# Kernel optimization log

Hardware: AMD Instinct MI355X
Metric: run time of the kernel (lower is better)

## Reference

```python
import jax, jax.numpy as jnp
import numpy as np

B, F, N, E, T = 8, 16, 1024, 256, 64
ALPHA = 0.2        # LeakyReLU negative slope
NEG = -9.0e15      # masking value used by the torch code


def setup_inputs() -> dict:
    key = jax.random.key(0)
    ks = jax.random.split(key, 9)
    x = jax.random.normal(ks[0], (B, F, N, T), dtype=jnp.float32)
    mask = (jax.random.uniform(ks[1], (B, F, N, T)) > 0.2).astype(jnp.float32)
    # binary incidence matrix [n_nodes, n_edges]; guarantee every hyperedge
    # has at least one incident node (avoids div-by-zero / empty softmax)
    inc = (jax.random.uniform(ks[2], (N, E)) < 0.05).astype(jnp.float32)
    inc = inc.at[0, :].set(1.0)
    h0 = jax.random.normal(ks[3], (1, N), dtype=jnp.float32)      # initial node state row
    h1 = jax.random.normal(ks[4], (E, 1), dtype=jnp.float32)      # initial edge state
    bias = jax.random.uniform(ks[5], (N,), dtype=jnp.float32)     # THGAT.bias (d_model == N)
    weight = jax.random.uniform(ks[6], (2 * F + 1,), dtype=jnp.float32)  # [3*d_in-ish, 1] proj
    weight2 = jax.random.uniform(ks[7], (E, E), dtype=jnp.float32) / E   # edge mixing
    a = jax.random.uniform(ks[8], (2,), dtype=jnp.float32)        # GAT attention vector
    return {"x": x, "mask": mask, "incidence": inc, "h0": h0, "h1": h1,
            "bias": bias, "weight": weight, "weight2": weight2, "a": a}


def _thgat_step(x_s, m_s, n_s, h_e, incidence, bias, weight, weight2, a):
    # x_s, m_s: [B,F,N]; n_s: [B,1,N]; h_e: [B,E,1]
    x_cat = jnp.concatenate([x_s, m_s, n_s], axis=1)          # [B,2F+1,N]
    xn = jnp.einsum('bcn,c->bn', x_cat, weight) + bias         # node feature (scalar per node)
    deg = jnp.sum(incidence, axis=0)                           # [E] hyperedge degree
    edge = (xn @ incidence) / deg                              # [B,E] mean of incident nodes
    edge = edge @ weight2                                      # [B,E]
    # pairwise GAT score at nonzero (n,e) pairs; computed densely then masked,
    # identical math to torch's gather -> sparse_coo -> to_dense path
    s = jax.nn.leaky_relu(xn[:, :, None] * a[0] + edge[:, None, :] * a[1], ALPHA)  # [B,N,E]
    time_e = h_e[:, :, 0] + edge                               # agg_type='sum': pri_e + edge
    s = s + time_e[:, None, :]
    att = jnp.where(incidence[None] > 0, s, NEG)
    attn = jax.nn.softmax(att, axis=1)                         # softmax over nodes per edge
    node = jnp.einsum('bne,be->bn', attn, edge)                # aggregate edge feats to nodes
    return node[:, None, :], edge[:, :, None]                  # [B,1,N], [B,E,1]


def reference(x, mask, incidence, h0, h1, bias, weight, weight2, a):
    n0 = jnp.broadcast_to(h0[None], (B, 1, N))
    e0 = jnp.broadcast_to(h1[None], (B, E, 1))
    xs = jnp.moveaxis(x, -1, 0)     # [T,B,F,N]
    ms = jnp.moveaxis(mask, -1, 0)

    def step(carry, inp):
        n_s, h_e = carry
        x_s, m_s = inp
        node, edge = _thgat_step(x_s, m_s, n_s, h_e, incidence, bias, weight, weight2, a)
        return (node, edge), node[:, 0, :]

    _, nodes = jax.lax.scan(step, (n0, e0), (xs, ms))
    return jnp.moveaxis(nodes, 0, 1)  # [B,T,N] imputations per timestep
```

## Files before the change

### kernel.cpp

```cpp
#include <hip/hip_runtime.h>

#define Bq 8
#define Fq 16
#define Nq 1024
#define Eq 256
#define Tq 64
constexpr float ALPHAq = 0.2f;
constexpr int NNZCAP = 32768;
constexpr int MAXJE  = 20;
constexpr int NNZW2  = 20480;
constexpr int DUMP0  = NNZW2;
constexpr int WVLTOT = NNZW2 + 1024;

__device__ __forceinline__ float qswap1(float x) {
  return __int_as_float(__builtin_amdgcn_mov_dpp(__float_as_int(x), 0xB1, 0xF, 0xF, true));
}
__device__ __forceinline__ float qswap2(float x) {
  return __int_as_float(__builtin_amdgcn_mov_dpp(__float_as_int(x), 0x4E, 0xF, 0xF, true));
}

__global__ __launch_bounds__(256) void k_cntB(const float* __restrict__ inc,
                                              int* __restrict__ gcnt,
                                              int* __restrict__ ncnt) {
  const int i = blockIdx.x, e = threadIdx.x;
  const int base = i * 64;
  int c = 0;
  for (int r = 0; r < 64; ++r) c += (inc[(size_t)(base + r) * Eq + e] > 0.f) ? 1 : 0;
  gcnt[i * Eq + e] = c;
  if (i < 4) {
    const int n = i * 256 + e;
    const float* row = inc + (size_t)n * Eq;
    int cn = 0;
    for (int k = 0; k < Eq; ++k) cn += (row[k] > 0.f) ? 1 : 0;
    ncnt[n] = cn;
  }
}

__global__ __launch_bounds__(1024) void k_prefB(const int* __restrict__ gcnt,
                                                const int* __restrict__ ncnt,
                                                int* __restrict__ g_ptr,
                                                int* __restrict__ goff,
                                                int* __restrict__ tlp,
                                                int* __restrict__ tlp2) {
  __shared__ int tot[Eq];
  __shared__ int sptr[Eq + 1];
  __shared__ int sn[Nq];
  __shared__ int snp[Nq + 1];
  __shared__ int snp2[Nq + 1];
  const int tid = threadIdx.x;
  if (tid < Eq) { int s = 0; for (int i = 0; i < 16; ++i) s += gcnt[i * Eq + tid]; tot[tid] = s; }
  sn[tid] = ncnt[tid];
  __syncthreads();
  if (tid == 0) { int s = 0; for (int j = 0; j < Eq; ++j) { sptr[j] = s; s += tot[j]; } sptr[Eq] = s; }
  if (tid == 1) { int s = 0; for (int i = 0; i < Nq; ++i) { snp[i] = s; s += sn[i]; } snp[Nq] = s; }
  if (tid == 2) { int s = 0; for (int i = 0; i < Nq; ++i) { snp2[i] = s; s += (sn[i] + 3) & ~3; } snp2[Nq] = s; }
  __syncthreads();
  if (tid <= Eq) g_ptr[tid] = sptr[tid];
  tlp[tid] = snp[tid];
  tlp2[tid] = snp2[tid];
  if (tid == 0) { tlp[Nq] = snp[Nq]; tlp2[Nq] = snp2[Nq]; }
  if (tid < Eq) {
    int run = sptr[tid];
    for (int i = 0; i < 16; ++i) { goff[i * Eq + tid] = run; run += gcnt[i * Eq + tid]; }
  }
}

__global__ __launch_bounds__(256) void k_fillB(const float* __restrict__ inc,
                                               const int* __restrict__ goff,
                                               const int* __restrict__ tlp,
                                               unsigned short* __restrict__ g_nodes,
                                               unsigned short* __restrict__ tle_g) {
  const int i = blockIdx.x, e = threadIdx.x;
  const int base = i * 64;
  int w = goff[i * Eq + e];
  for (int r = 0; r < 64; ++r) {
    const int n = base + r;
    if (inc[(size_t)n * Eq + e] > 0.f) { if (w < NNZCAP) g_nodes[w] = (unsigned short)n; ++w; }
  }
  if (i < 4) {
    const int n = i * 256 + e;
    const float* row = inc + (size_t)n * Eq;
    int wn = tlp[n];
    for (int k = 0; k < Eq; ++k)
      if (row[k] > 0.f) { if (wn < NNZCAP) tle_g[wn] = (unsigned short)k; ++wn; }
  }
}

__global__ __launch_bounds__(256) void k_prep(const int* __restrict__ g_ptr,
                                              const unsigned short* __restrict__ g_nodes,
                                              const int* __restrict__ tlp_g,
                                              const int* __restrict__ tlp2_g,
                                              const unsigned short* __restrict__ tle_g,
                                              unsigned* __restrict__ tbl_g,
                                              unsigned short* __restrict__ wpos_g) {
  const int t = blockIdx.x * 256 + threadIdx.x;
  const int e = t >> 2, sub = t & 3;
  const int p0 = g_ptr[e], p1 = g_ptr[e + 1];
  int j = 0;
  for (int pos = p0 + sub; pos < p1; pos += 4, ++j) {
    const int n = (int)g_nodes[pos];
    int lo = tlp_g[n], hi = tlp_g[n + 1];
    while (lo < hi) { int mid = (lo + hi) >> 1; if ((int)tle_g[mid] < e) lo = mid + 1; else hi = mid; }
    int wp = tlp2_g[n] + (lo - tlp_g[n]);
    if (wp >= NNZW2) wp = DUMP0 + t;
    wpos_g[pos] = (unsigned short)wp;
    if (j < MAXJE) tbl_g[j * Nq + t] = ((unsigned)wp << 16) | (unsigned)n;
  }
  for (; j < MAXJE; ++j)
    tbl_g[j * Nq + t] = ((unsigned)(DUMP0 + t) << 16) | (unsigned)Nq;
}

__global__ __launch_bounds__(256) void k_xnp(const float* __restrict__ x,
                                             const float* __restrict__ mask,
                                             const float* __restrict__ weight,
                                             const float* __restrict__ bias,
                                             float* __restrict__ xnpT) {
  __shared__ float accs[64][65];
  const int wg = blockIdx.x;
  const int b = wg >> 4;
  const int n0 = (wg & 15) << 6;
  const int lane = threadIdx.x & 63;
  const int w = threadIdx.x >> 6;
  float a[16];
#pragma unroll
  for (int i = 0; i < 16; ++i) a[i] = 0.f;
  for (int f = 0; f < Fq; ++f) {
    const float wf = weight[f], wm = weight[Fq + f];
#pragma unroll
    for (int ii = 0; ii < 16; ++ii) {
      const int i = w + ii * 4;
      const size_t base = ((size_t)(b * Fq + f) * Nq + n0 + i) * Tq + lane;
      a[ii] += x[base] * wf + mask[base] * wm;
    }
  }
#pragma unroll
  for (int ii = 0; ii < 16; ++ii) accs[w + ii * 4][lane] = a[ii];
  __syncthreads();
  const float bl = bias[n0 + lane];
#pragma unroll
  for (int jj = 0; jj < 16; ++jj) {
    const int tt = w + jj * 4;
    xnpT[((size_t)b * Tq + tt) * Nq + n0 + lane] = accs[lane][tt] + bl;
  }
}

__global__ __attribute__((amdgpu_flat_work_group_size(1024, 1024), amdgpu_waves_per_eu(4, 4)))
void k_recur(
    const float* __restrict__ xnpT, const float* __restrict__ w2,
    const int* __restrict__ g_ptr, const unsigned short* __restrict__ g_nodes,
    const unsigned short* __restrict__ wpos_g,
    const int* __restrict__ tlp_g, const int* __restrict__ tlp2_g,
    const unsigned* __restrict__ tbl_g,
    const float* __restrict__ h0,
    const float* __restrict__ weight, const float* __restrict__ a_vec,
    float* __restrict__ out) {
  __shared__ __align__(16) float wvl[WVLTOT];
  __shared__ float xnl[Nq + 4];
  __shared__ __align__(16) float epp[4 * 72];

  const int b = blockIdx.x;
  const int tid = threadIdx.x;
  const int e = tid >> 2;
  const int sub = tid & 3;
  const float w32 = weight[2 * Fq];
  const float a0 = a_vec[0], a1 = a_vec[1];

  for (int i = tid; i < WVLTOT; i += 1024) wvl[i] = 0.f;

  float xn_reg = xnpT[(size_t)b * Tq * Nq + tid] + w32 * h0[tid];
  xnl[tid] = xn_reg;
  if (tid == 0) xnl[Nq] = 0.f;

  unsigned uj[MAXJE];
#pragma unroll
  for (int j = 0; j < MAXJE; ++j) uj[j] = tbl_g[j * Nq + tid];

  float w2r[64];
#pragma unroll
  for (int kk = 0; kk < 64; ++kk)
    w2r[kk] = w2[(size_t)(sub * 64 + kk) * Eq + e];

  const int p0 = g_ptr[e], p1 = g_ptr[e + 1];
  const float degf = (float)(p1 - p0);
  const int tail0 = p0 + sub + 4 * MAXJE;
  const int q0v = tlp2_g[tid] >> 2;
  const int degn = tlp_g[tid + 1] - tlp_g[tid];
  const int iters = (tid == 0) ? 0 : ((degn + 3) >> 2);
  __syncthreads();

  float xv[MAXJE];

  for (int t = 0; t < Tq; ++t) {
    const float xnext = xnpT[((size_t)b * Tq + (t + 1 < Tq ? t + 1 : t)) * Nq + tid];

    float v = 0.f;
    float mxv = -3.0e38f;
#pragma unroll
    for (int j = 0; j < MAXJE; ++j) {
      const int n = (int)(uj[j] & 0xffffu);
      const float xx = xnl[n];
      v += xx;
      const float val = (n < Nq) ? xx : -1.0e30f;
      xv[j] = val;
      mxv = fmaxf(mxv, val);
    }
    for (int pos = tail0; pos < p1; pos += 4) {
      const float xx = xnl[(int)g_nodes[pos]];
      v += xx;
      mxv = fmaxf(mxv, xx);
    }
    v += qswap1(v);
    v += qswap2(v);
    mxv = fmaxf(mxv, qswap1(mxv));
    mxv = fmaxf(mxv, qswap2(mxv));
    if (sub == 0) epp[(e >> 6) * 72 + (e & 63)] = v / degf;
    __syncthreads();

    float acc = 0.f;
#pragma unroll
    for (int k = 0; k < 16; ++k) {
      const float4 epv = *reinterpret_cast<const float4*>(&epp[sub * 72 + (k << 2)]);
      acc += w2r[k * 4 + 0] * epv.x + w2r[k * 4 + 1] * epv.y +
             w2r[k * 4 + 2] * epv.z + w2r[k * 4 + 3] * epv.w;
    }
    acc += qswap1(acc);
    acc += qswap2(acc);
    const float edge2 = acc;
    const float e2a1 = edge2 * a1;
    const float sm = mxv * a0 + e2a1;
    const float mx = fmaxf(sm, ALPHAq * sm);

    float Zs = 0.f;
#pragma unroll
    for (int j = 0; j < MAXJE; ++j) {
      const float s = xv[j] * a0 + e2a1;
      const float p = __expf(fmaxf(s, ALPHAq * s) - mx);
      xv[j] = p;
      Zs += p;
    }
    for (int pos = tail0; pos < p1; pos += 4) {
      const float s = xnl[(int)g_nodes[pos]] * a0 + e2a1;
      Zs += __expf(fmaxf(s, ALPHAq * s) - mx);
    }
    Zs += qswap1(Zs);
    Zs += qswap2(Zs);
    const float we = edge2 / Zs;

#pragma unroll
    for (int j = 0; j < MAXJE; ++j)
      wvl[uj[j] >> 16] = xv[j] * we;
    for (int pos = tail0; pos < p1; pos += 4) {
      const float s = xnl[(int)g_nodes[pos]] * a0 + e2a1;
      wvl[(int)wpos_g[pos]] = __expf(fmaxf(s, ALPHAq * s) - mx) * we;
    }
    __syncthreads();

    float nv = 0.f;
    if (tid < 64) {
      const float4 w4 = reinterpret_cast<const float4*>(wvl)[tid];
      float q = w4.x + w4.y + w4.z + w4.w;
#pragma unroll
      for (int m = 32; m > 0; m >>= 1) q += __shfl_xor(q, m);
      if (tid == 0) nv = q;
    }
    for (int i = 0; i < iters; ++i) {
      const float4 w4 = reinterpret_cast<const float4*>(wvl)[q0v + i];
      nv += w4.x + w4.y + w4.z + w4.w;
    }

    out[((size_t)b * Tq + t) * Nq + tid] = nv;
    xn_reg = xnext + w32 * nv;
    xnl[tid] = xn_reg;
    __syncthreads();
  }
}

extern "C" void kernel_launch(void* const* d_in, const int* in_sizes, int n_in,
                              void* d_out, int out_size, void* d_ws, size_t ws_size,
                              hipStream_t stream) {
  (void)in_sizes; (void)n_in; (void)out_size; (void)ws_size;
  const float* x      = (const float*)d_in[0];
  const float* mask   = (const float*)d_in[1];
  const float* inc    = (const float*)d_in[2];
  const float* h0     = (const float*)d_in[3];
  const float* bias   = (const float*)d_in[5];
  const float* weight = (const float*)d_in[6];
  const float* w2     = (const float*)d_in[7];
  const float* avec   = (const float*)d_in[8];
  float* out = (float*)d_out;

  char* ws = (char*)d_ws;
  size_t off = 0;
  auto alloc = [&](size_t bytes) { void* p = ws + off; off += (bytes + 255) & ~(size_t)255; return p; };
  int*            g_ptr   = (int*)alloc((Eq + 1) * 4);
  int*            gcnt    = (int*)alloc(16 * Eq * 4);
  int*            goff    = (int*)alloc(16 * Eq * 4);
  unsigned short* g_nodes = (unsigned short*)alloc((size_t)NNZCAP * 2);
  int*            ncnt    = (int*)alloc(Nq * 4);
  int*            tlp_g   = (int*)alloc((Nq + 1) * 4);
  int*            tlp2_g  = (int*)alloc((Nq + 1) * 4);
  unsigned short* tle_g   = (unsigned short*)alloc((size_t)NNZCAP * 2);
  unsigned short* wpos_g  = (unsigned short*)alloc((size_t)NNZCAP * 2);
  unsigned*       tbl_g   = (unsigned*)alloc((size_t)MAXJE * Nq * 4);
  float*          xnpT    = (float*)alloc((size_t)Bq * Tq * Nq * 4);

  k_cntB <<<16, 256, 0, stream>>>(inc, gcnt, ncnt);
  k_prefB<<<1, 1024, 0, stream>>>(gcnt, ncnt, g_ptr, goff, tlp_g, tlp2_g);
  k_fillB<<<16, 256, 0, stream>>>(inc, goff, tlp_g, g_nodes, tle_g);
  k_prep <<<4, 256, 0, stream>>>(g_ptr, g_nodes, tlp_g, tlp2_g, tle_g, tbl_g, wpos_g);
  k_xnp  <<<128, 256, 0, stream>>>(x, mask, weight, bias, xnpT);
  k_recur<<<Bq, 1024, 0, stream>>>(xnpT, w2, g_ptr, g_nodes, wpos_g, tlp_g, tlp2_g,
                                   tbl_g, h0, weight, avec, out);
}
```

Baseline: 549.3 us.

## Sort hyperedges by degree and skip unused padded slots per wave

Hyperedges are ranked by degree in the prefix kernel, and each thread quad is mapped to an edge through that ranking. Edges with similar degree therefore share a wavefront. The recurrence computes a wave-uniform maximum slot count and skips padded MAXJE slots in the gather, exp and scatter loops. This cuts wasted LDS loads and exps in the latency-bound per-timestep loop, at the cost of an extra indirection, a scalar branch per slot, and an O(E²) rank computation during setup.

```diff
diff --git a/kernel.cpp b/kernel.cpp
--- a/kernel.cpp
+++ b/kernel.cpp
@@ -41,7 +41,8 @@
                                                 int* __restrict__ g_ptr,
                                                 int* __restrict__ goff,
                                                 int* __restrict__ tlp,
-                                                int* __restrict__ tlp2) {
+                                                int* __restrict__ tlp2,
+                                                unsigned short* __restrict__ eq_g) {
   __shared__ int tot[Eq];
   __shared__ int sptr[Eq + 1];
   __shared__ int sn[Nq];
@@ -63,6 +64,15 @@
     int run = sptr[tid];
     for (int i = 0; i < 16; ++i) { goff[i * Eq + tid] = run; run += gcnt[i * Eq + tid]; }
   }
+  if (tid < Eq) {
+    const int d = tot[tid];
+    int r = 0;
+    for (int e2 = 0; e2 < Eq; ++e2) {
+      const int d2 = tot[e2];
+      r += (d2 > d) || (d2 == d && e2 < tid);
+    }
+    eq_g[r] = (unsigned short)tid;
+  }
 }
 
 __global__ __launch_bounds__(256) void k_fillB(const float* __restrict__ inc,
@@ -91,10 +101,12 @@
                                               const int* __restrict__ tlp_g,
                                               const int* __restrict__ tlp2_g,
                                               const unsigned short* __restrict__ tle_g,
+                                              const unsigned short* __restrict__ eq_g,
                                               unsigned* __restrict__ tbl_g,
                                               unsigned short* __restrict__ wpos_g) {
   const int t = blockIdx.x * 256 + threadIdx.x;
-  const int e = t >> 2, sub = t & 3;
+  const int q = t >> 2, sub = t & 3;
+  const int e = (int)eq_g[q];
   const int p0 = g_ptr[e], p1 = g_ptr[e + 1];
   int j = 0;
   for (int pos = p0 + sub; pos < p1; pos += 4, ++j) {
@@ -150,7 +162,7 @@
     const int* __restrict__ g_ptr, const unsigned short* __restrict__ g_nodes,
     const unsigned short* __restrict__ wpos_g,
     const int* __restrict__ tlp_g, const int* __restrict__ tlp2_g,
-    const unsigned* __restrict__ tbl_g,
+    const unsigned* __restrict__ tbl_g, const unsigned short* __restrict__ eq_g,
     const float* __restrict__ h0,
     const float* __restrict__ weight, const float* __restrict__ a_vec,
     float* __restrict__ out) {
@@ -160,8 +172,9 @@
 
   const int b = blockIdx.x;
   const int tid = threadIdx.x;
-  const int e = tid >> 2;
+  const int q = tid >> 2;
   const int sub = tid & 3;
+  const int e = (int)eq_g[q];
   const float w32 = weight[2 * Fq];
   const float a0 = a_vec[0], a1 = a_vec[1];
 
@@ -181,11 +194,19 @@
     w2r[kk] = w2[(size_t)(sub * 64 + kk) * Eq + e];
 
   const int p0 = g_ptr[e], p1 = g_ptr[e + 1];
-  const float degf = (float)(p1 - p0);
+  const int deg = p1 - p0;
+  const float degf = (float)deg;
   const int tail0 = p0 + sub + 4 * MAXJE;
   const int q0v = tlp2_g[tid] >> 2;
   const int degn = tlp_g[tid + 1] - tlp_g[tid];
   const int iters = (tid == 0) ? 0 : ((degn + 3) >> 2);
+
+  int cnt = (deg - sub + 3) >> 2;
+  int cm = cnt;
+#pragma unroll
+  for (int m = 1; m <= 32; m <<= 1) { const int o = __shfl_xor(cm, m); cm = (o > cm) ? o : cm; }
+  cm = __builtin_amdgcn_readfirstlane(cm);
+  if (cm > MAXJE) cm = MAXJE;
   __syncthreads();
 
   float xv[MAXJE];
@@ -197,12 +218,14 @@
     float mxv = -3.0e38f;
 #pragma unroll
     for (int j = 0; j < MAXJE; ++j) {
-      const int n = (int)(uj[j] & 0xffffu);
-      const float xx = xnl[n];
-      v += xx;
-      const float val = (n < Nq) ? xx : -1.0e30f;
-      xv[j] = val;
-      mxv = fmaxf(mxv, val);
+      if (j < cm) {
+        const int n = (int)(uj[j] & 0xffffu);
+        const float xx = xnl[n];
+        v += xx;
+        const float val = (n < Nq) ? xx : -1.0e30f;
+        xv[j] = val;
+        mxv = fmaxf(mxv, val);
+      }
     }
     for (int pos = tail0; pos < p1; pos += 4) {
       const float xx = xnl[(int)g_nodes[pos]];
@@ -233,10 +256,12 @@
     float Zs = 0.f;
 #pragma unroll
     for (int j = 0; j < MAXJE; ++j) {
-      const float s = xv[j] * a0 + e2a1;
-      const float p = __expf(fmaxf(s, ALPHAq * s) - mx);
-      xv[j] = p;
-      Zs += p;
+      if (j < cm) {
+        const float s = xv[j] * a0 + e2a1;
+        const float p = __expf(fmaxf(s, ALPHAq * s) - mx);
+        xv[j] = p;
+        Zs += p;
+      }
     }
     for (int pos = tail0; pos < p1; pos += 4) {
       const float s = xnl[(int)g_nodes[pos]] * a0 + e2a1;
@@ -247,8 +272,10 @@
     const float we = edge2 / Zs;
 
 #pragma unroll
-    for (int j = 0; j < MAXJE; ++j)
-      wvl[uj[j] >> 16] = xv[j] * we;
+    for (int j = 0; j < MAXJE; ++j) {
+      if (j < cm)
+        wvl[uj[j] >> 16] = xv[j] * we;
+    }
     for (int pos = tail0; pos < p1; pos += 4) {
       const float s = xnl[(int)g_nodes[pos]] * a0 + e2a1;
       wvl[(int)wpos_g[pos]] = __expf(fmaxf(s, ALPHAq * s) - mx) * we;
@@ -258,10 +285,10 @@
     float nv = 0.f;
     if (tid < 64) {
       const float4 w4 = reinterpret_cast<const float4*>(wvl)[tid];
-      float q = w4.x + w4.y + w4.z + w4.w;
-#pragma unroll
-      for (int m = 32; m > 0; m >>= 1) q += __shfl_xor(q, m);
-      if (tid == 0) nv = q;
+      float qv = w4.x + w4.y + w4.z + w4.w;
+#pragma unroll
+      for (int m = 32; m > 0; m >>= 1) qv += __shfl_xor(qv, m);
+      if (tid == 0) nv = qv;
     }
     for (int i = 0; i < iters; ++i) {
       const float4 w4 = reinterpret_cast<const float4*>(wvl)[q0v + i];
@@ -301,14 +328,15 @@
   int*            tlp2_g  = (int*)alloc((Nq + 1) * 4);
   unsigned short* tle_g   = (unsigned short*)alloc((size_t)NNZCAP * 2);
   unsigned short* wpos_g  = (unsigned short*)alloc((size_t)NNZCAP * 2);
+  unsigned short* eq_g    = (unsigned short*)alloc(Eq * 2);
   unsigned*       tbl_g   = (unsigned*)alloc((size_t)MAXJE * Nq * 4);
   float*          xnpT    = (float*)alloc((size_t)Bq * Tq * Nq * 4);
 
   k_cntB <<<16, 256, 0, stream>>>(inc, gcnt, ncnt);
-  k_prefB<<<1, 1024, 0, stream>>>(gcnt, ncnt, g_ptr, goff, tlp_g, tlp2_g);
+  k_prefB<<<1, 1024, 0, stream>>>(gcnt, ncnt, g_ptr, goff, tlp_g, tlp2_g, eq_g);
   k_fillB<<<16, 256, 0, stream>>>(inc, goff, tlp_g, g_nodes, tle_g);
-  k_prep <<<4, 256, 0, stream>>>(g_ptr, g_nodes, tlp_g, tlp2_g, tle_g, tbl_g, wpos_g);
+  k_prep <<<4, 256, 0, stream>>>(g_ptr, g_nodes, tlp_g, tlp2_g, tle_g, eq_g, tbl_g, wpos_g);
   k_xnp  <<<128, 256, 0, stream>>>(x, mask, weight, bias, xnpT);
   k_recur<<<Bq, 1024, 0, stream>>>(xnpT, w2, g_ptr, g_nodes, wpos_g, tlp_g, tlp2_g,
-                                   tbl_g, h0, weight, avec, out);
-}
+                                   tbl_g, eq_g, h0, weight, avec, out);
+}
```

Result: slower. 582.7 us (+6.1%).
